# Performance work log

Measured on AMD Instinct MI355X. Metric: run time of the kernel, lower is better.

The kernel has to match this reference:

```python
import jax, jax.numpy as jnp
import numpy as np
import math

N, B, T, E = 4, 8, 2, 1024
H, D = 16, 64
S, L = 2048, 1024
NB = N * B

def setup_inputs() -> dict:
    key = jax.random.key(0)
    ks = jax.random.split(key, 10)
    sc = 0.02
    return {
        'hidden_states': jax.random.normal(ks[0], (NB, T, E), jnp.float32),
        'attention_mask': jnp.zeros((NB, 1, 1, S + L + T), jnp.float32),
        'past_prefix_key': jax.random.normal(ks[1], (N, H, S, D), jnp.float32),
        'past_prefix_value': jax.random.normal(ks[2], (N, H, S, D), jnp.float32),
        'past_key': jax.random.normal(ks[3], (NB, H, L, D), jnp.float32),
        'past_value': jax.random.normal(ks[4], (NB, H, L, D), jnp.float32),
        'Wq': jax.random.normal(ks[5], (E, E), jnp.float32) * sc,
        'bq': jnp.zeros((E,), jnp.float32),
        'Wk': jax.random.normal(ks[6], (E, E), jnp.float32) * sc,
        'bk': jnp.zeros((E,), jnp.float32),
        'Wv': jax.random.normal(ks[7], (E, E), jnp.float32) * sc,
        'bv': jnp.zeros((E,), jnp.float32),
    }

def _heads(x):
    # (NB, T, E) -> (NB, H, T, D)
    return x.reshape(NB, T, H, D).transpose(0, 2, 1, 3)

def reference(hidden_states, attention_mask, past_prefix_key, past_prefix_value,
              past_key, past_value, Wq, bq, Wk, bk, Wv, bv):
    scale = 1.0 / math.sqrt(D)
    q = _heads(hidden_states @ Wq.T + bq)   # (NB,H,T,D)
    k_new = _heads(hidden_states @ Wk.T + bk)
    v_new = _heads(hidden_states @ Wv.T + bv)

    # prefix scores: broadcast shared prefix KV across beams
    q_beam = q.reshape(N, B, H, T, D)
    prefix_scores = jnp.einsum('bxhtd,bhsd->bxhts', q_beam, past_prefix_key)
    prefix_scores = prefix_scores.reshape(NB, H, T, S) * scale

    # current KV = cached target prefix + new tokens
    k = jnp.concatenate([past_key, k_new], axis=2)   # (NB,H,L+T,D)
    v = jnp.concatenate([past_value, v_new], axis=2)
    cur_scores = jnp.einsum('bhtd,bhsd->bhts', q, k) * scale

    scores = jnp.concatenate([prefix_scores, cur_scores], axis=-1) + attention_mask
    probs = jax.nn.softmax(scores, axis=-1)          # (NB,H,T,S+L+T)

    prefix_probs = probs[..., :S].reshape(N, B, H, T, S)
    cur_probs = probs[..., S:]
    prefix_ctx = jnp.einsum('bxhts,bhsd->bxhtd', prefix_probs, past_prefix_value)
    prefix_ctx = prefix_ctx.reshape(NB, H, T, D)
    ctx = prefix_ctx + jnp.einsum('bhts,bhsd->bhtd', cur_probs, v)

    # (NB,H,T,D) -> (NB,T,E)
    return ctx.transpose(0, 2, 1, 3).reshape(NB, T, H * D)
```

## Files before the change

### kernel.cpp

```cpp
#include <hip/hip_runtime.h>
#include <hip/hip_bf16.h>

#define NB_  32
#define T_   2
#define E_   1024
#define H_   16
#define D_   64
#define S_   2048
#define L_   1024
#define TOT_ (S_ + L_ + T_)

#define PCH_  16
#define PLEN_ (S_ / PCH_)
#define NT_   8
#define PFXU_ (4 * H_ * PCH_)

#define LOG2E_ 1.4426950408889634f
#define QS_ (0.125f * LOG2E_)

#define GLOAD_LDS16(g, l) __builtin_amdgcn_global_load_lds( \
    (const __attribute__((address_space(1))) void*)(g), \
    (__attribute__((address_space(3))) void*)(l), 16, 0, 0)

__global__ __launch_bounds__(256) void qkv_kernel(
    const float* __restrict__ hidden,
    const float* __restrict__ Wq, const float* __restrict__ bq,
    const float* __restrict__ Wk, const float* __restrict__ bk,
    const float* __restrict__ Wv, const float* __restrict__ bv,
    float* __restrict__ qT,
    float* __restrict__ knew,
    float* __restrict__ vnew)
{
    __shared__ float ldsT[128 * 65];
    __shared__ float wlds[8 * 128];
    const int tid  = threadIdx.x;
    const int wave = tid >> 6;
    const int lane = tid & 63;
    const int eg0  = blockIdx.x * 8;
    const int mat  = eg0 >> 10;
    const int e0   = eg0 & 1023;
    int c0 = wave * 2;
    c0 = __builtin_amdgcn_readfirstlane(c0);

    const float* W    = (mat == 0) ? Wq : (mat == 1) ? Wk : Wv;
    const float* bias = (mat == 0) ? bq : (mat == 1) ? bk : bv;

    float aA0 = 0.f, aB0 = 0.f, aA1 = 0.f, aB1 = 0.f;

    for (int k0 = 0; k0 < 1024; k0 += 128) {
        __syncthreads();
        #pragma unroll
        for (int i = 0; i < 32; i++) {
            int f = i * 256 + tid;
            int r = f >> 7;
            int c = f & 127;
            ldsT[c * 65 + r] = hidden[r * 1024 + k0 + c];
        }
        {
            int wr = tid >> 5;
            int wc = (tid & 31) * 4;
            *reinterpret_cast<float4*>(&wlds[wr * 128 + wc]) =
                *reinterpret_cast<const float4*>(&W[(size_t)(e0 + wr) * 1024 + k0 + wc]);
        }
        __syncthreads();

        for (int kk = 0; kk < 128; kk += 4) {
            float h0 = ldsT[(kk + 0) * 65 + lane];
            float h1 = ldsT[(kk + 1) * 65 + lane];
            float h2 = ldsT[(kk + 2) * 65 + lane];
            float h3 = ldsT[(kk + 3) * 65 + lane];
            float4 w0 = *reinterpret_cast<const float4*>(&wlds[(c0 + 0) * 128 + kk]);
            float4 w1 = *reinterpret_cast<const float4*>(&wlds[(c0 + 1) * 128 + kk]);
            aA0 = fmaf(h0, w0.x, aA0); aA0 = fmaf(h1, w0.y, aA0);
            aB0 = fmaf(h2, w0.z, aB0); aB0 = fmaf(h3, w0.w, aB0);
            aA1 = fmaf(h0, w1.x, aA1); aA1 = fmaf(h1, w1.y, aA1);
            aB1 = fmaf(h2, w1.z, aB1); aB1 = fmaf(h3, w1.w, aB1);
        }
    }

    const int r = lane;
    #pragma unroll
    for (int j = 0; j < 2; j++) {
        int e_in = e0 + c0 + j;
        float val = ((j == 0) ? (aA0 + aB0) : (aA1 + aB1)) + bias[e_in];
        if (mat == 0) {
            qT[e_in * 64 + r] = val;
        } else {
            int nb = r >> 1, t = r & 1, h = e_in >> 6, d = e_in & 63;
            float* dst = (mat == 1) ? knew : vnew;
            dst[((nb * H_ + h) * T_ + t) * D_ + d] = val;
        }
    }
}

__global__ __launch_bounds__(1024) void cur_kernel(
    const float* __restrict__ mask,
    const float* __restrict__ pk,
    const float* __restrict__ pv,
    const float* __restrict__ qT,
    const float* __restrict__ knew,
    const float* __restrict__ vnew,
    float* __restrict__ cur_ctx,
    float* __restrict__ cur_l)
{
    __shared__ float part_acc[64][128];
    __shared__ float part_l[64][2];

    const int bid = blockIdx.x;
    const int nb  = bid >> 4;
    const int h   = bid & 15;

    const int tid = threadIdx.x;
    const int G   = tid >> 4;
    const int l16 = tid & 15;
    const int d0  = l16 * 4;

    float qf0[4], qf1[4];
    #pragma unroll
    for (int j = 0; j < 4; j++) {
        const float* qb = qT + (h * 64 + d0 + j) * 64 + nb * 2;
        qf0[j] = qb[0] * QS_;
        qf1[j] = qb[1] * QS_;
    }

    const float* pk_b = pk + ((nb * H_ + h) * (size_t)L_) * D_;
    const float* pv_b = pv + ((nb * H_ + h) * (size_t)L_) * D_;
    const float* kn_b = knew + (nb * H_ + h) * (T_ * D_);
    const float* vn_b = vnew + (nb * H_ + h) * (T_ * D_);
    const float* mrow = mask + nb * TOT_ + S_;

    float l0 = 0.f, l1 = 0.f;
    float a0[4] = {0.f, 0.f, 0.f, 0.f};
    float a1[4] = {0.f, 0.f, 0.f, 0.f};

    for (int p = G; p < L_ + T_; p += 64) {
        const float* kp;
        const float* vp;
        if (p < L_) { kp = pk_b + p * D_;        vp = pv_b + p * D_; }
        else        { kp = kn_b + (p - L_) * D_; vp = vn_b + (p - L_) * D_; }

        float4 kf = *reinterpret_cast<const float4*>(kp + d0);
        float s0 = qf0[0] * kf.x + qf0[1] * kf.y + qf0[2] * kf.z + qf0[3] * kf.w;
        float s1 = qf1[0] * kf.x + qf1[1] * kf.y + qf1[2] * kf.z + qf1[3] * kf.w;
        #pragma unroll
        for (int off = 1; off < 16; off <<= 1) {
            s0 += __shfl_xor(s0, off, 64);
            s1 += __shfl_xor(s1, off, 64);
        }
        float mC = mrow[p] * LOG2E_;
        float e0 = exp2f(s0 + mC);
        float e1 = exp2f(s1 + mC);
        l0 += e0;
        l1 += e1;
        float4 vf = *reinterpret_cast<const float4*>(vp + d0);
        a0[0] += e0 * vf.x; a0[1] += e0 * vf.y; a0[2] += e0 * vf.z; a0[3] += e0 * vf.w;
        a1[0] += e1 * vf.x; a1[1] += e1 * vf.y; a1[2] += e1 * vf.z; a1[3] += e1 * vf.w;
    }

    if (l16 == 0) { part_l[G][0] = l0; part_l[G][1] = l1; }
    #pragma unroll
    for (int j = 0; j < 4; j++) {
        part_acc[G][d0 + j]      = a0[j];
        part_acc[G][64 + d0 + j] = a1[j];
    }
    __syncthreads();

    if (tid < 128) {
        int t = tid >> 6, d = tid & 63;
        float s = 0.f, l = 0.f;
        for (int g = 0; g < 64; g++) {
            s += part_acc[g][t * 64 + d];
            l += part_l[g][t];
        }
        cur_ctx[(bid * 2 + t) * 64 + d] = s;
        if (d == 0) cur_l[bid * 2 + t] = l;
    }
}

__global__ __launch_bounds__(256) void pfx_partial_kernel(
    const float* __restrict__ mask,
    const float* __restrict__ pfx_k,
    const float* __restrict__ pfx_v,
    const float* __restrict__ qT,
    float* __restrict__ pfx_ctx,
    float* __restrict__ pfx_l)
{
    __shared__ float smem[4160];
    const int tid = threadIdx.x;

    const int v     = blockIdx.x;
    const int n     = v >> 8;
    const int h     = (v >> 4) & 15;
    const int chunk = v & 15;
    const int wv    = tid >> 6;
    const int lane  = tid & 63;
    const int r     = lane & 15;
    const int c     = lane >> 4;

    float qreg[16];
    const float* qbase = qT + (h * 64 + c * 16) * 64 + (n * 16 + r);
    #pragma unroll
    for (int u = 0; u < 16; u++) qreg[u] = qbase[u * 64] * QS_;

    const size_t pos0 = (size_t)(n * H_ + h) * S_ + chunk * PLEN_;
    const float* kb = pfx_k + pos0 * D_;
    const float* vb = pfx_v + pos0 * D_;
    const float* mrow = mask + (n * 8 + (r >> 1)) * TOT_ + chunk * PLEN_;

    float ctx[16];
    #pragma unroll
    for (int u = 0; u < 16; u++) ctx[u] = 0.f;
    float lsum = 0.f;

    GLOAD_LDS16(kb + tid * 4, &smem[tid * 4]);
    GLOAD_LDS16(vb + tid * 4, &smem[1024 + tid * 4]);

    #pragma unroll 1
    for (int t = 0; t < NT_; t++) {
        const int bufo = (t & 1) * 2048;
        __syncthreads();

        float mreg[4];
        #pragma unroll
        for (int j = 0; j < 4; j++)
            mreg[j] = mrow[t * 16 + wv * 4 + j] * LOG2E_;

        if (t < NT_ - 1) {
            const int nbo = ((t + 1) & 1) * 2048;
            const float* kn = kb + (size_t)(t + 1) * 16 * 64;
            const float* vn = vb + (size_t)(t + 1) * 16 * 64;
            GLOAD_LDS16(kn + tid * 4, &smem[nbo + tid * 4]);
            GLOAD_LDS16(vn + tid * 4, &smem[nbo + 1024 + tid * 4]);
        }

        #pragma unroll
        for (int j = 0; j < 4; j++) {
            const int pp = wv * 4 + j;
            const float4* kq = reinterpret_cast<const float4*>(
                &smem[bufo + pp * 64 + c * 16]);
            float4 k0 = kq[0], k1 = kq[1], k2 = kq[2], k3 = kq[3];
            float sA = qreg[0]*k0.x;  sA = fmaf(qreg[1],k0.y,sA);
            sA = fmaf(qreg[2],k0.z,sA); sA = fmaf(qreg[3],k0.w,sA);
            float sB = qreg[4]*k1.x;  sB = fmaf(qreg[5],k1.y,sB);
            sB = fmaf(qreg[6],k1.z,sB); sB = fmaf(qreg[7],k1.w,sB);
            float sC = qreg[8]*k2.x;  sC = fmaf(qreg[9],k2.y,sC);
            sC = fmaf(qreg[10],k2.z,sC); sC = fmaf(qreg[11],k2.w,sC);
            float sD = qreg[12]*k3.x; sD = fmaf(qreg[13],k3.y,sD);
            sD = fmaf(qreg[14],k3.z,sD); sD = fmaf(qreg[15],k3.w,sD);
            float s = (sA + sB) + (sC + sD);
            s += __shfl_xor(s, 16, 64);
            s += __shfl_xor(s, 32, 64);
            float e = exp2f(s + mreg[j]);
            lsum += e;
            const float4* vq = reinterpret_cast<const float4*>(
                &smem[bufo + 1024 + pp * 64 + c * 16]);
            float4 v0 = vq[0], v1 = vq[1], v2 = vq[2], v3 = vq[3];
            ctx[0]  += e * v0.x; ctx[1]  += e * v0.y; ctx[2]  += e * v0.z; ctx[3]  += e * v0.w;
            ctx[4]  += e * v1.x; ctx[5]  += e * v1.y; ctx[6]  += e * v1.z; ctx[7]  += e * v1.w;
            ctx[8]  += e * v2.x; ctx[9]  += e * v2.y; ctx[10] += e * v2.z; ctx[11] += e * v2.w;
            ctx[12] += e * v3.x; ctx[13] += e * v3.y; ctx[14] += e * v3.z; ctx[15] += e * v3.w;
        }
    }

    __syncthreads();
    const int base = wv * 1024 + r * 64 + c * 16;
    #pragma unroll
    for (int u = 0; u < 16; u += 4)
        *reinterpret_cast<float4*>(&smem[base + u]) =
            make_float4(ctx[u], ctx[u+1], ctx[u+2], ctx[u+3]);
    if (c == 0) smem[4096 + wv * 16 + r] = lsum;
    __syncthreads();

    const int pc = (n * H_ + h) * PCH_ + chunk;
    for (int e = tid; e < 1024; e += 256) {
        float s = smem[e] + smem[1024 + e] + smem[2048 + e] + smem[3072 + e];
        pfx_ctx[pc * 1024 + e] = s;
    }
    if (tid < 16) {
        float l = smem[4096 + tid] + smem[4096 + 16 + tid]
                + smem[4096 + 32 + tid] + smem[4096 + 48 + tid];
        pfx_l[pc * 16 + tid] = l;
    }
}

__global__ __launch_bounds__(256) void combine_kernel(
    const float* __restrict__ cur_ctx, const float* __restrict__ cur_l,
    const float* __restrict__ pfx_ctx, const float* __restrict__ pfx_l,
    float* __restrict__ out)
{
    const int row = blockIdx.x >> 2;
    const int qtr = blockIdx.x & 3;
    const int nb  = row >> 1, t = row & 1;
    const int n   = nb >> 3;
    const int r   = (nb & 7) * 2 + t;
    const int e   = qtr * 256 + threadIdx.x;
    const int h   = e >> 6, d = e & 63;
    const int b   = nb * 16 + h;

    float val = cur_ctx[(b * 2 + t) * 64 + d];
    float l   = cur_l[b * 2 + t];
    #pragma unroll
    for (int ch = 0; ch < PCH_; ch++) {
        int pc = (n * H_ + h) * PCH_ + ch;
        val += pfx_ctx[pc * 1024 + r * 64 + d];
        l   += pfx_l[pc * 16 + r];
    }
    out[row * 1024 + e] = val / l;
}

extern "C" void kernel_launch(void* const* d_in, const int* in_sizes, int n_in,
                              void* d_out, int out_size, void* d_ws, size_t ws_size,
                              hipStream_t stream) {
    const float* hidden = (const float*)d_in[0];
    const float* mask   = (const float*)d_in[1];
    const float* pfxk   = (const float*)d_in[2];
    const float* pfxv   = (const float*)d_in[3];
    const float* pk     = (const float*)d_in[4];
    const float* pv     = (const float*)d_in[5];
    const float* Wq     = (const float*)d_in[6];
    const float* bq     = (const float*)d_in[7];
    const float* Wk     = (const float*)d_in[8];
    const float* bk     = (const float*)d_in[9];
    const float* Wv     = (const float*)d_in[10];
    const float* bv     = (const float*)d_in[11];

    float* qT      = (float*)d_ws;
    float* knew    = qT + 65536;
    float* vnew    = knew + 65536;
    float* cur_ctx = vnew + 65536;
    float* cur_l   = cur_ctx + 65536;
    float* pfx_ctx = cur_l + 1024;
    float* pfx_l   = pfx_ctx + 1048576;

    qkv_kernel<<<384, 256, 0, stream>>>(hidden, Wq, bq, Wk, bk, Wv, bv,
                                        qT, knew, vnew);
    cur_kernel<<<512, 1024, 0, stream>>>(
        mask, pk, pv, qT, knew, vnew, cur_ctx, cur_l);
    pfx_partial_kernel<<<PFXU_, 256, 0, stream>>>(
        mask, pfxk, pfxv, qT, pfx_ctx, pfx_l);
    combine_kernel<<<256, 256, 0, stream>>>(cur_ctx, cur_l, pfx_ctx, pfx_l,
                                            (float*)d_out);
}
```

Measured before the change: 111.6 us.

## Stream cached KV through a triple-buffered LDS ring with async global-to-LDS loads

Rewrites the per-(beam,head) current-KV attention kernel to use 256 threads. It streams the 1024 cached K/V rows in 32-row tiles into a 3-slot LDS ring via global_load_lds, with explicit vmcnt waits and barriers so loads overlap compute. The mask row is also preloaded into LDS, and the reduction is shrunk from 64 to 16 groups. The aim is to hide HBM latency for this bandwidth-bound stream, with fewer threads and less reduction work. The trade-off is lower thread-level parallelism per block and reliance on manual waitcnt correctness.

```diff
diff --git a/kernel.cpp b/kernel.cpp
--- a/kernel.cpp
+++ b/kernel.cpp
@@ -14,6 +14,12 @@
 #define PLEN_ (S_ / PCH_)
 #define NT_   8
 #define PFXU_ (4 * H_ * PCH_)
+
+#define CTILE_ 32
+#define NTIL_  (L_ / CTILE_)
+#define RING_  3
+#define SLOTF_ 4096
+#define MOFF_  (RING_ * SLOTF_)
 
 #define LOG2E_ 1.4426950408889634f
 #define QS_ (0.125f * LOG2E_)
@@ -93,7 +99,7 @@
     }
 }
 
-__global__ __launch_bounds__(1024) void cur_kernel(
+__global__ __launch_bounds__(256) void cur_stream_kernel(
     const float* __restrict__ mask,
     const float* __restrict__ pk,
     const float* __restrict__ pv,
@@ -103,15 +109,12 @@
     float* __restrict__ cur_ctx,
     float* __restrict__ cur_l)
 {
-    __shared__ float part_acc[64][128];
-    __shared__ float part_l[64][2];
-
+    __shared__ float smem[MOFF_ + 1056];
+    const int tid = threadIdx.x;
     const int bid = blockIdx.x;
     const int nb  = bid >> 4;
     const int h   = bid & 15;
-
-    const int tid = threadIdx.x;
-    const int G   = tid >> 4;
+    const int g   = tid >> 4;
     const int l16 = tid & 15;
     const int d0  = l16 * 4;
 
@@ -125,52 +128,112 @@
 
     const float* pk_b = pk + ((nb * H_ + h) * (size_t)L_) * D_;
     const float* pv_b = pv + ((nb * H_ + h) * (size_t)L_) * D_;
-    const float* kn_b = knew + (nb * H_ + h) * (T_ * D_);
-    const float* vn_b = vnew + (nb * H_ + h) * (T_ * D_);
     const float* mrow = mask + nb * TOT_ + S_;
 
+    for (int i = tid; i < L_ + T_; i += 256)
+        smem[MOFF_ + i] = mrow[i] * LOG2E_;
+    __syncthreads();
+
     float l0 = 0.f, l1 = 0.f;
-    float a0[4] = {0.f, 0.f, 0.f, 0.f};
-    float a1[4] = {0.f, 0.f, 0.f, 0.f};
-
-    for (int p = G; p < L_ + T_; p += 64) {
-        const float* kp;
-        const float* vp;
-        if (p < L_) { kp = pk_b + p * D_;        vp = pv_b + p * D_; }
-        else        { kp = kn_b + (p - L_) * D_; vp = vn_b + (p - L_) * D_; }
-
-        float4 kf = *reinterpret_cast<const float4*>(kp + d0);
-        float s0 = qf0[0] * kf.x + qf0[1] * kf.y + qf0[2] * kf.z + qf0[3] * kf.w;
-        float s1 = qf1[0] * kf.x + qf1[1] * kf.y + qf1[2] * kf.z + qf1[3] * kf.w;
+    float a0[4] = {0.f,0.f,0.f,0.f};
+    float a1[4] = {0.f,0.f,0.f,0.f};
+
+    auto stage_tile = [&](int t, int s) {
+        const float* kt = pk_b + (size_t)t * (CTILE_ * D_);
+        const float* vt = pv_b + (size_t)t * (CTILE_ * D_);
+        GLOAD_LDS16(kt + tid * 4,        &smem[s * SLOTF_ + tid * 4]);
+        GLOAD_LDS16(kt + 1024 + tid * 4, &smem[s * SLOTF_ + 1024 + tid * 4]);
+        GLOAD_LDS16(vt + tid * 4,        &smem[s * SLOTF_ + 2048 + tid * 4]);
+        GLOAD_LDS16(vt + 1024 + tid * 4, &smem[s * SLOTF_ + 3072 + tid * 4]);
+    };
+
+    auto compute_tile = [&](int t, int s) {
+        #pragma unroll
+        for (int sub = 0; sub < 2; sub++) {
+            const int pl = sub * 16 + g;
+            float4 kf = *reinterpret_cast<const float4*>(
+                &smem[s * SLOTF_ + pl * 64 + d0]);
+            float s0 = fmaf(qf0[0],kf.x, qf0[1]*kf.y) + fmaf(qf0[2],kf.z, qf0[3]*kf.w);
+            float s1 = fmaf(qf1[0],kf.x, qf1[1]*kf.y) + fmaf(qf1[2],kf.z, qf1[3]*kf.w);
+            #pragma unroll
+            for (int off = 1; off < 16; off <<= 1) {
+                s0 += __shfl_xor(s0, off, 64);
+                s1 += __shfl_xor(s1, off, 64);
+            }
+            float mC = smem[MOFF_ + t * CTILE_ + pl];
+            float e0 = exp2f(s0 + mC);
+            float e1 = exp2f(s1 + mC);
+            l0 += e0; l1 += e1;
+            float4 vf = *reinterpret_cast<const float4*>(
+                &smem[s * SLOTF_ + 2048 + pl * 64 + d0]);
+            a0[0] += e0 * vf.x; a0[1] += e0 * vf.y; a0[2] += e0 * vf.z; a0[3] += e0 * vf.w;
+            a1[0] += e1 * vf.x; a1[1] += e1 * vf.y; a1[2] += e1 * vf.z; a1[3] += e1 * vf.w;
+        }
+    };
+
+    stage_tile(0, 0);
+    stage_tile(1, 1);
+    stage_tile(2, 2);
+
+    #pragma unroll 1
+    for (int t = 0; t < NTIL_ - 3; t++) {
+        asm volatile("s_waitcnt vmcnt(8)" ::: "memory");
+        __builtin_amdgcn_sched_barrier(0);
+        __builtin_amdgcn_s_barrier();
+        compute_tile(t, t % RING_);
+        __builtin_amdgcn_s_barrier();
+        stage_tile(t + 3, t % RING_);
+    }
+    asm volatile("s_waitcnt vmcnt(8)" ::: "memory");
+    __builtin_amdgcn_sched_barrier(0);
+    __builtin_amdgcn_s_barrier();
+    compute_tile(29, 29 % RING_);
+    __builtin_amdgcn_s_barrier();
+    asm volatile("s_waitcnt vmcnt(4)" ::: "memory");
+    __builtin_amdgcn_sched_barrier(0);
+    __builtin_amdgcn_s_barrier();
+    compute_tile(30, 30 % RING_);
+    __builtin_amdgcn_s_barrier();
+    asm volatile("s_waitcnt vmcnt(0)" ::: "memory");
+    __builtin_amdgcn_sched_barrier(0);
+    __builtin_amdgcn_s_barrier();
+    compute_tile(31, 31 % RING_);
+
+    if (g < 2) {
+        const float* kn_b = knew + (nb * H_ + h) * (T_ * D_);
+        const float* vn_b = vnew + (nb * H_ + h) * (T_ * D_);
+        float4 kfn = *reinterpret_cast<const float4*>(kn_b + g * D_ + d0);
+        float s0 = fmaf(qf0[0],kfn.x, qf0[1]*kfn.y) + fmaf(qf0[2],kfn.z, qf0[3]*kfn.w);
+        float s1 = fmaf(qf1[0],kfn.x, qf1[1]*kfn.y) + fmaf(qf1[2],kfn.z, qf1[3]*kfn.w);
         #pragma unroll
         for (int off = 1; off < 16; off <<= 1) {
             s0 += __shfl_xor(s0, off, 64);
             s1 += __shfl_xor(s1, off, 64);
         }
-        float mC = mrow[p] * LOG2E_;
+        float mC = smem[MOFF_ + L_ + g];
         float e0 = exp2f(s0 + mC);
         float e1 = exp2f(s1 + mC);
-        l0 += e0;
-        l1 += e1;
-        float4 vf = *reinterpret_cast<const float4*>(vp + d0);
-        a0[0] += e0 * vf.x; a0[1] += e0 * vf.y; a0[2] += e0 * vf.z; a0[3] += e0 * vf.w;
-        a1[0] += e1 * vf.x; a1[1] += e1 * vf.y; a1[2] += e1 * vf.z; a1[3] += e1 * vf.w;
-    }
-
-    if (l16 == 0) { part_l[G][0] = l0; part_l[G][1] = l1; }
+        l0 += e0; l1 += e1;
+        float4 vfn = *reinterpret_cast<const float4*>(vn_b + g * D_ + d0);
+        a0[0] += e0 * vfn.x; a0[1] += e0 * vfn.y; a0[2] += e0 * vfn.z; a0[3] += e0 * vfn.w;
+        a1[0] += e1 * vfn.x; a1[1] += e1 * vfn.y; a1[2] += e1 * vfn.z; a1[3] += e1 * vfn.w;
+    }
+
+    __syncthreads();
     #pragma unroll
     for (int j = 0; j < 4; j++) {
-        part_acc[G][d0 + j]      = a0[j];
-        part_acc[G][64 + d0 + j] = a1[j];
-    }
+        smem[g * 128 + d0 + j]      = a0[j];
+        smem[g * 128 + 64 + d0 + j] = a1[j];
+    }
+    if (l16 == 0) { smem[2048 + g * 2] = l0; smem[2048 + g * 2 + 1] = l1; }
     __syncthreads();
 
     if (tid < 128) {
         int t = tid >> 6, d = tid & 63;
         float s = 0.f, l = 0.f;
-        for (int g = 0; g < 64; g++) {
-            s += part_acc[g][t * 64 + d];
-            l += part_l[g][t];
+        for (int g2 = 0; g2 < 16; g2++) {
+            s += smem[g2 * 128 + t * 64 + d];
+            l += smem[2048 + g2 * 2 + t];
         }
         cur_ctx[(bid * 2 + t) * 64 + d] = s;
         if (d == 0) cur_l[bid * 2 + t] = l;
@@ -334,7 +397,7 @@
 
     qkv_kernel<<<384, 256, 0, stream>>>(hidden, Wq, bq, Wk, bk, Wv, bv,
                                         qT, knew, vnew);
-    cur_kernel<<<512, 1024, 0, stream>>>(
+    cur_stream_kernel<<<512, 256, 0, stream>>>(
         mask, pk, pv, qT, knew, vnew, cur_ctx, cur_l);
     pfx_partial_kernel<<<PFXU_, 256, 0, stream>>>(
         mask, pfxk, pfxv, qT, pfx_ctx, pfx_l);
```

Measured after the change: 111.8 us. No clear change (+0.2%).

## Split current-KV attention into 4 chunks with LDS-staged tiles and prefetch

Applied to the files above, without the earlier changes.

The current-token attention kernel changes from 512 blocks of 1024 threads to 2048 blocks of 256 threads, each handling a 256-position chunk. Each wave stages 16-position K/V tiles into LDS (K transposed and padded) while register-prefetching the next tile, then computes scores and the PV accumulation from LDS. The two new tokens are handled by the last chunk, and the combine kernel now sums the four chunk partials. The aim is more parallelism and better-coalesced, overlapped memory traffic, at the cost of a larger workspace and extra partial reads.

```diff
diff --git a/kernel.cpp b/kernel.cpp
--- a/kernel.cpp
+++ b/kernel.cpp
@@ -14,6 +14,17 @@
 #define PLEN_ (S_ / PCH_)
 #define NT_   8
 #define PFXU_ (4 * H_ * PCH_)
+
+#define CCH2_  4
+#define CPOS2_ 256
+#define PERW_  2144
+#define VOFF_  1088
+#define EOFF_  2112
+#define MOFF2_ (4 * PERW_)
+#define QOFF_  (MOFF2_ + 264)
+#define TBOFF_ (QOFF_ + 128)
+#define LTOFF_ (TBOFF_ + 256)
+#define SMEM2_ 9232
 
 #define LOG2E_ 1.4426950408889634f
 #define QS_ (0.125f * LOG2E_)
@@ -93,7 +104,7 @@
     }
 }
 
-__global__ __launch_bounds__(1024) void cur_kernel(
+__global__ __launch_bounds__(256) void cur_gemm_kernel(
     const float* __restrict__ mask,
     const float* __restrict__ pk,
     const float* __restrict__ pv,
@@ -103,77 +114,169 @@
     float* __restrict__ cur_ctx,
     float* __restrict__ cur_l)
 {
-    __shared__ float part_acc[64][128];
-    __shared__ float part_l[64][2];
-
-    const int bid = blockIdx.x;
-    const int nb  = bid >> 4;
-    const int h   = bid & 15;
-
-    const int tid = threadIdx.x;
-    const int G   = tid >> 4;
-    const int l16 = tid & 15;
-    const int d0  = l16 * 4;
-
-    float qf0[4], qf1[4];
-    #pragma unroll
-    for (int j = 0; j < 4; j++) {
-        const float* qb = qT + (h * 64 + d0 + j) * 64 + nb * 2;
-        qf0[j] = qb[0] * QS_;
-        qf1[j] = qb[1] * QS_;
-    }
-
-    const float* pk_b = pk + ((nb * H_ + h) * (size_t)L_) * D_;
-    const float* pv_b = pv + ((nb * H_ + h) * (size_t)L_) * D_;
-    const float* kn_b = knew + (nb * H_ + h) * (T_ * D_);
-    const float* vn_b = vnew + (nb * H_ + h) * (T_ * D_);
-    const float* mrow = mask + nb * TOT_ + S_;
-
-    float l0 = 0.f, l1 = 0.f;
-    float a0[4] = {0.f, 0.f, 0.f, 0.f};
-    float a1[4] = {0.f, 0.f, 0.f, 0.f};
-
-    for (int p = G; p < L_ + T_; p += 64) {
-        const float* kp;
-        const float* vp;
-        if (p < L_) { kp = pk_b + p * D_;        vp = pv_b + p * D_; }
-        else        { kp = kn_b + (p - L_) * D_; vp = vn_b + (p - L_) * D_; }
-
-        float4 kf = *reinterpret_cast<const float4*>(kp + d0);
-        float s0 = qf0[0] * kf.x + qf0[1] * kf.y + qf0[2] * kf.z + qf0[3] * kf.w;
-        float s1 = qf1[0] * kf.x + qf1[1] * kf.y + qf1[2] * kf.z + qf1[3] * kf.w;
+    __shared__ float smem[SMEM2_];
+    const int tid   = threadIdx.x;
+    const int u     = blockIdx.x;
+    const int b     = u >> 2;
+    const int chunk = u & 3;
+    const int nb    = b >> 4;
+    const int h     = b & 15;
+    const int w     = tid >> 6;
+    const int l     = tid & 63;
+    const int p16   = l & 15;
+    const int dq    = l >> 4;
+
+    const float* pk_b = pk + ((nb * H_ + h) * (size_t)L_ + chunk * CPOS2_) * D_;
+    const float* pv_b = pv + ((nb * H_ + h) * (size_t)L_ + chunk * CPOS2_) * D_;
+    const float* mrow = mask + nb * TOT_ + S_ + chunk * CPOS2_;
+
+    for (int i = tid; i < CPOS2_; i += 256)
+        smem[MOFF2_ + i] = mrow[i] * LOG2E_;
+    if (chunk == 3 && tid < 2)
+        smem[MOFF2_ + CPOS2_ + tid] = mrow[CPOS2_ + tid] * LOG2E_;
+    if (tid < 64) {
+        float q0 = qT[(h * 64 + tid) * 64 + nb * 2];
+        float q1 = qT[(h * 64 + tid) * 64 + nb * 2 + 1];
+        smem[QOFF_ + tid * 2]     = q0 * QS_;
+        smem[QOFF_ + tid * 2 + 1] = q1 * QS_;
+    }
+    __syncthreads();
+
+    float* WR = smem + w * PERW_;
+
+    float ctx0 = 0.f, ctx1 = 0.f, lw0 = 0.f, lw1 = 0.f;
+    float4 kr0, kr1, kr2, kr3, vr0, vr1, vr2, vr3;
+
+    {
+        const float* kt = pk_b + (size_t)w * 1024;
+        const float* vt = pv_b + (size_t)w * 1024;
+        kr0 = *reinterpret_cast<const float4*>(kt + 0   + l * 4);
+        kr1 = *reinterpret_cast<const float4*>(kt + 256 + l * 4);
+        kr2 = *reinterpret_cast<const float4*>(kt + 512 + l * 4);
+        kr3 = *reinterpret_cast<const float4*>(kt + 768 + l * 4);
+        vr0 = *reinterpret_cast<const float4*>(vt + 0   + l * 4);
+        vr1 = *reinterpret_cast<const float4*>(vt + 256 + l * 4);
+        vr2 = *reinterpret_cast<const float4*>(vt + 512 + l * 4);
+        vr3 = *reinterpret_cast<const float4*>(vt + 768 + l * 4);
+    }
+
+    #pragma unroll 1
+    for (int i = 0; i < 4; i++) {
+        const int tile = w + i * 4;
+
+        {
+            const int d0 = (l & 15) * 4;
+            const int pb = l >> 4;
+            WR[(d0+0)*17 + (pb+ 0)] = kr0.x; WR[(d0+1)*17 + (pb+ 0)] = kr0.y;
+            WR[(d0+2)*17 + (pb+ 0)] = kr0.z; WR[(d0+3)*17 + (pb+ 0)] = kr0.w;
+            WR[(d0+0)*17 + (pb+ 4)] = kr1.x; WR[(d0+1)*17 + (pb+ 4)] = kr1.y;
+            WR[(d0+2)*17 + (pb+ 4)] = kr1.z; WR[(d0+3)*17 + (pb+ 4)] = kr1.w;
+            WR[(d0+0)*17 + (pb+ 8)] = kr2.x; WR[(d0+1)*17 + (pb+ 8)] = kr2.y;
+            WR[(d0+2)*17 + (pb+ 8)] = kr2.z; WR[(d0+3)*17 + (pb+ 8)] = kr2.w;
+            WR[(d0+0)*17 + (pb+12)] = kr3.x; WR[(d0+1)*17 + (pb+12)] = kr3.y;
+            WR[(d0+2)*17 + (pb+12)] = kr3.z; WR[(d0+3)*17 + (pb+12)] = kr3.w;
+            *reinterpret_cast<float4*>(&WR[VOFF_ + (pb+ 0)*64 + d0]) = vr0;
+            *reinterpret_cast<float4*>(&WR[VOFF_ + (pb+ 4)*64 + d0]) = vr1;
+            *reinterpret_cast<float4*>(&WR[VOFF_ + (pb+ 8)*64 + d0]) = vr2;
+            *reinterpret_cast<float4*>(&WR[VOFF_ + (pb+12)*64 + d0]) = vr3;
+        }
+
+        if (i < 3) {
+            const float* kt = pk_b + (size_t)(tile + 4) * 1024;
+            const float* vt = pv_b + (size_t)(tile + 4) * 1024;
+            kr0 = *reinterpret_cast<const float4*>(kt + 0   + l * 4);
+            kr1 = *reinterpret_cast<const float4*>(kt + 256 + l * 4);
+            kr2 = *reinterpret_cast<const float4*>(kt + 512 + l * 4);
+            kr3 = *reinterpret_cast<const float4*>(kt + 768 + l * 4);
+            vr0 = *reinterpret_cast<const float4*>(vt + 0   + l * 4);
+            vr1 = *reinterpret_cast<const float4*>(vt + 256 + l * 4);
+            vr2 = *reinterpret_cast<const float4*>(vt + 512 + l * 4);
+            vr3 = *reinterpret_cast<const float4*>(vt + 768 + l * 4);
+        }
+
+        float s0 = 0.f, s1 = 0.f;
+        #pragma unroll
+        for (int dd = 0; dd < 16; dd++) {
+            float  kv = WR[(dq * 16 + dd) * 17 + p16];
+            float2 q  = *reinterpret_cast<const float2*>(
+                            &smem[QOFF_ + (dq * 16 + dd) * 2]);
+            s0 = fmaf(kv, q.x, s0);
+            s1 = fmaf(kv, q.y, s1);
+        }
+        s0 += __shfl_xor(s0, 16, 64); s0 += __shfl_xor(s0, 32, 64);
+        s1 += __shfl_xor(s1, 16, 64); s1 += __shfl_xor(s1, 32, 64);
+        float mC = smem[MOFF2_ + tile * 16 + p16];
+        float e0 = exp2f(s0 + mC);
+        float e1 = exp2f(s1 + mC);
+        if (dq == 0)
+            *reinterpret_cast<float2*>(&WR[EOFF_ + p16 * 2]) = make_float2(e0, e1);
+
+        #pragma unroll
+        for (int pp = 0; pp < 16; pp++) {
+            float2 e = *reinterpret_cast<const float2*>(&WR[EOFF_ + pp * 2]);
+            float  v = WR[VOFF_ + pp * 64 + l];
+            ctx0 = fmaf(e.x, v, ctx0);
+            ctx1 = fmaf(e.y, v, ctx1);
+            lw0 += e.x; lw1 += e.y;
+        }
+    }
+
+    WR[l]      = ctx0;
+    WR[64 + l] = ctx1;
+    if (l == 0) { WR[128] = lw0; WR[129] = lw1; }
+
+    if (chunk == 3 && w == 0 && dq < 2) {
+        const float* kn_b = knew + (nb * H_ + h) * (T_ * D_);
+        const float* vn_b = vnew + (nb * H_ + h) * (T_ * D_);
+        const int d0 = p16 * 4;
+        float4 kfn = *reinterpret_cast<const float4*>(kn_b + dq * 64 + d0);
+        float s0 = 0.f, s1 = 0.f;
+        #pragma unroll
+        for (int j = 0; j < 4; j++) {
+            float2 q = *reinterpret_cast<const float2*>(&smem[QOFF_ + (d0 + j) * 2]);
+            float kv = (j == 0) ? kfn.x : (j == 1) ? kfn.y : (j == 2) ? kfn.z : kfn.w;
+            s0 = fmaf(kv, q.x, s0);
+            s1 = fmaf(kv, q.y, s1);
+        }
         #pragma unroll
         for (int off = 1; off < 16; off <<= 1) {
             s0 += __shfl_xor(s0, off, 64);
             s1 += __shfl_xor(s1, off, 64);
         }
-        float mC = mrow[p] * LOG2E_;
+        float mC = smem[MOFF2_ + CPOS2_ + dq];
         float e0 = exp2f(s0 + mC);
         float e1 = exp2f(s1 + mC);
-        l0 += e0;
-        l1 += e1;
-        float4 vf = *reinterpret_cast<const float4*>(vp + d0);
-        a0[0] += e0 * vf.x; a0[1] += e0 * vf.y; a0[2] += e0 * vf.z; a0[3] += e0 * vf.w;
-        a1[0] += e1 * vf.x; a1[1] += e1 * vf.y; a1[2] += e1 * vf.z; a1[3] += e1 * vf.w;
-    }
-
-    if (l16 == 0) { part_l[G][0] = l0; part_l[G][1] = l1; }
-    #pragma unroll
-    for (int j = 0; j < 4; j++) {
-        part_acc[G][d0 + j]      = a0[j];
-        part_acc[G][64 + d0 + j] = a1[j];
+        float4 vfn = *reinterpret_cast<const float4*>(vn_b + dq * 64 + d0);
+        smem[TBOFF_ + (dq * 2 + 0) * 64 + d0 + 0] = e0 * vfn.x;
+        smem[TBOFF_ + (dq * 2 + 0) * 64 + d0 + 1] = e0 * vfn.y;
+        smem[TBOFF_ + (dq * 2 + 0) * 64 + d0 + 2] = e0 * vfn.z;
+        smem[TBOFF_ + (dq * 2 + 0) * 64 + d0 + 3] = e0 * vfn.w;
+        smem[TBOFF_ + (dq * 2 + 1) * 64 + d0 + 0] = e1 * vfn.x;
+        smem[TBOFF_ + (dq * 2 + 1) * 64 + d0 + 1] = e1 * vfn.y;
+        smem[TBOFF_ + (dq * 2 + 1) * 64 + d0 + 2] = e1 * vfn.z;
+        smem[TBOFF_ + (dq * 2 + 1) * 64 + d0 + 3] = e1 * vfn.w;
+        if (p16 == 0) {
+            smem[LTOFF_ + dq * 2 + 0] = e0;
+            smem[LTOFF_ + dq * 2 + 1] = e1;
+        }
     }
     __syncthreads();
 
     if (tid < 128) {
-        int t = tid >> 6, d = tid & 63;
-        float s = 0.f, l = 0.f;
-        for (int g = 0; g < 64; g++) {
-            s += part_acc[g][t * 64 + d];
-            l += part_l[g][t];
-        }
-        cur_ctx[(bid * 2 + t) * 64 + d] = s;
-        if (d == 0) cur_l[bid * 2 + t] = l;
+        const int t = tid >> 6, d = tid & 63;
+        float s = 0.f, lv = 0.f;
+        #pragma unroll
+        for (int w2 = 0; w2 < 4; w2++) {
+            s  += smem[w2 * PERW_ + t * 64 + d];
+            lv += smem[w2 * PERW_ + 128 + t];
+        }
+        if (chunk == 3) {
+            s  += smem[TBOFF_ + (0 * 2 + t) * 64 + d]
+                + smem[TBOFF_ + (1 * 2 + t) * 64 + d];
+            lv += smem[LTOFF_ + 0 * 2 + t] + smem[LTOFF_ + 1 * 2 + t];
+        }
+        cur_ctx[(u * 2 + t) * 64 + d] = s;
+        if (d == 0) cur_l[u * 2 + t] = lv;
     }
 }
 
@@ -297,8 +400,13 @@
     const int h   = e >> 6, d = e & 63;
     const int b   = nb * 16 + h;
 
-    float val = cur_ctx[(b * 2 + t) * 64 + d];
-    float l   = cur_l[b * 2 + t];
+    float val = 0.f, l = 0.f;
+    #pragma unroll
+    for (int ch = 0; ch < CCH2_; ch++) {
+        int cb = b * CCH2_ + ch;
+        val += cur_ctx[(cb * 2 + t) * 64 + d];
+        l   += cur_l[cb * 2 + t];
+    }
     #pragma unroll
     for (int ch = 0; ch < PCH_; ch++) {
         int pc = (n * H_ + h) * PCH_ + ch;
@@ -328,13 +436,13 @@
     float* knew    = qT + 65536;
     float* vnew    = knew + 65536;
     float* cur_ctx = vnew + 65536;
-    float* cur_l   = cur_ctx + 65536;
-    float* pfx_ctx = cur_l + 1024;
+    float* cur_l   = cur_ctx + 262144;
+    float* pfx_ctx = cur_l + 4096;
     float* pfx_l   = pfx_ctx + 1048576;
 
     qkv_kernel<<<384, 256, 0, stream>>>(hidden, Wq, bq, Wk, bk, Wv, bv,
                                         qT, knew, vnew);
-    cur_kernel<<<512, 1024, 0, stream>>>(
+    cur_gemm_kernel<<<NB_ * H_ * CCH2_, 256, 0, stream>>>(
         mask, pk, pv, qT, knew, vnew, cur_ctx, cur_l);
     pfx_partial_kernel<<<PFXU_, 256, 0, stream>>>(
         mask, pfxk, pfxv, qT, pfx_ctx, pfx_l);
```

Measured after the change: 107.1 us. -4.0%, faster.
